# Optimization experiments

Measured on AMD Instinct MI355X. Metric: run time of the kernel, lower is better.

Reference implementation:

```python
import jax, jax.numpy as jnp
import numpy as np

B, N, E, DIN, DH = 32, 2000, 64000, 128, 128


def setup_inputs() -> dict:
    key = jax.random.key(0)
    ks = jax.random.split(key, 8)
    gene_emb = jax.random.normal(ks[0], (B, N, DIN), dtype=jnp.float32)
    edge_src = jax.random.randint(ks[1], (E,), 0, N, dtype=jnp.int32)
    edge_dst = jax.random.randint(ks[2], (E,), 0, N, dtype=jnp.int32)
    s1 = 1.0 / np.sqrt(DIN)
    s2 = 1.0 / np.sqrt(DH)
    W1 = jax.random.normal(ks[3], (DIN, DH), dtype=jnp.float32) * s1
    b1 = jnp.zeros((DH,), dtype=jnp.float32)
    W2 = jax.random.normal(ks[4], (DH, DH), dtype=jnp.float32) * s2
    b2 = jnp.zeros((DH,), dtype=jnp.float32)
    return {"gene_emb": gene_emb, "edge_src": edge_src, "edge_dst": edge_dst,
            "W1": W1, "b1": b1, "W2": W2, "b2": b2, "pathway_idx": 0}


def _gcn_conv(x, src, dst, norm_e, self_norm, W, b):
    # x: [B, N, Din] -> [B, N, Dout]; PyG GCNConv: linear first, then normalized aggregation
    h = jnp.einsum('bnd,de->bne', x, W)
    msgs = h[:, src, :] * norm_e[None, :, None]          # [B, E, Dout] gather
    agg = jax.vmap(lambda m: jax.ops.segment_sum(m, dst, num_segments=h.shape[1]))(msgs)
    # self-loop contribution (A+I): norm = dinv[i]^2
    return agg + h * self_norm[None, :, None] + b


def reference(gene_emb, edge_src, edge_dst, W1, b1, W2, b2, pathway_idx):
    n = gene_emb.shape[1]
    # symmetric GCN normalization with self loops: deg[i] = in_degree + 1
    deg = jnp.zeros((n,), dtype=gene_emb.dtype).at[edge_dst].add(1.0) + 1.0
    dinv = jax.lax.rsqrt(deg)
    norm_e = dinv[edge_src] * dinv[edge_dst]
    self_norm = dinv * dinv
    x = jax.nn.relu(_gcn_conv(gene_emb, edge_src, edge_dst, norm_e, self_norm, W1, b1))
    x = _gcn_conv(x, edge_src, edge_dst, norm_e, self_norm, W2, b2)
    # global_mean_pool over each graph copy (all graphs have n nodes)
    return jnp.mean(x, axis=1)  # [B, DH]
```

## Files before the change

### kernel.cpp

```cpp
#include <hip/hip_runtime.h>

namespace {
constexpr int NB = 32;
constexpr int NN = 2000;
constexpr int NE = 64000;
constexpr int ND = 128;
constexpr int TR = 16;
constexpr int NCHUNK = NN / TR;
constexpr int NXCD = 8;
constexpr int BPB = 2;
constexpr int PAIRS_PER_XCD = NB / (NXCD * BPB);
constexpr int NPAIR = NB / BPB;
constexpr int GRID_FUSED = NPAIR * NCHUNK;
constexpr int SL = 80;

constexpr int CVT_BLOCKS  = 1000;
constexpr int W_BLOCKS    = 8;
constexpr int EDGE_BLOCKS = 250;

constexpr size_t OFF_CNT    = 0;
constexpr size_t OFF_CNT2   = 8192;
constexpr size_t OFF_WSUM   = 16384;
constexpr size_t MEMSET_BYTES = 24576;
constexpr size_t OFF_SLOT2  = 24576;
constexpr size_t OFF_WF     = OFF_SLOT2 + (size_t)NN * SL * 8;
constexpr size_t OFF_YP     = OFF_WF + 32768;
constexpr size_t OFF_XBF    = OFF_YP + (size_t)NB * NCHUNK * ND * 4;

typedef __attribute__((ext_vector_type(8))) short bf16x8;
typedef __attribute__((ext_vector_type(4))) float f32x4;

__device__ __forceinline__ ushort f32_to_bf16(float f) {
    uint u = __float_as_uint(f);
    u += 0x7fffu + ((u >> 16) & 1u);
    return (ushort)(u >> 16);
}
__device__ __forceinline__ uint pack_bf16x2(float lo, float hi) {
    return (uint)f32_to_bf16(lo) | ((uint)f32_to_bf16(hi) << 16);
}
}

__global__ void k_prep1(const float* __restrict__ X, ushort* __restrict__ xbf,
                        const float* __restrict__ W1, uint* __restrict__ wf,
                        const int* __restrict__ dst, int* __restrict__ cnt) {
    const int blk = blockIdx.x;
    if (blk < CVT_BLOCKS) {
        const float4* __restrict__ X4 = (const float4*)X;
        ushort4* __restrict__ O4 = (ushort4*)xbf;
        const int base = blk * 2048 + (int)threadIdx.x;
        #pragma unroll
        for (int k = 0; k < 8; k++) {
            int i = base + k * 256;
            float4 v = X4[i];
            ushort4 o;
            o.x = f32_to_bf16(v.x);
            o.y = f32_to_bf16(v.y);
            o.z = f32_to_bf16(v.z);
            o.w = f32_to_bf16(v.w);
            O4[i] = o;
        }
    } else if (blk < CVT_BLOCKS + W_BLOCKS) {
        int g = (blk - CVT_BLOCKS) * 256 + threadIdx.x;
        int lane = g & 63, f = g >> 6;
        int nt = f >> 2, kc = f & 3;
        int col = nt * 16 + (lane & 15);
        int k0  = kc * 32 + (lane >> 4) * 8;
        uint4 o;
        o.x = pack_bf16x2(W1[(k0 + 0) * ND + col], W1[(k0 + 1) * ND + col]);
        o.y = pack_bf16x2(W1[(k0 + 2) * ND + col], W1[(k0 + 3) * ND + col]);
        o.z = pack_bf16x2(W1[(k0 + 4) * ND + col], W1[(k0 + 5) * ND + col]);
        o.w = pack_bf16x2(W1[(k0 + 6) * ND + col], W1[(k0 + 7) * ND + col]);
        ((uint4*)wf)[g] = o;
    } else {
        int e = (blk - CVT_BLOCKS - W_BLOCKS) * 256 + threadIdx.x;
        atomicAdd(&cnt[dst[e]], 1);
    }
}

__global__ void k_prep2(const int* __restrict__ src, const int* __restrict__ dst,
                        const int* __restrict__ cnt, int* __restrict__ cnt2,
                        float* __restrict__ wsum, int2* __restrict__ slot2) {
    int e = blockIdx.x * 256 + threadIdx.x;
    int s = src[e], d = dst[e];
    float w = rsqrtf((float)(cnt[s] + 1)) * rsqrtf((float)(cnt[d] + 1));
    int p = atomicAdd(&cnt2[d], 1);
    if (p < SL) slot2[(size_t)d * SL + p] = make_int2(s, __float_as_int(w));
    atomicAdd(&wsum[s], w);
}

__global__ __launch_bounds__(256, 4) void k_fused(const ushort* __restrict__ xbf,
                                                  const int* __restrict__ cnt,
                                                  const int2* __restrict__ slot2,
                                                  const float* __restrict__ wsum,
                                                  const uint* __restrict__ wfrag,
                                                  const float* __restrict__ b1,
                                                  float* __restrict__ ypart) {
    __shared__ __align__(16) uint AsU[2][TR * 68];
    __shared__ int2  sE[TR][SL];
    __shared__ float sDinv[TR];
    __shared__ float sWn[TR];
    __shared__ int   sCnt[TR];
    const int tid = threadIdx.x;

    const int L     = blockIdx.x;
    const int xcd   = L & (NXCD - 1);
    const int sl    = L >> 3;
    const int pair  = sl / NCHUNK;
    const int chunk = sl - pair * NCHUNK;
    const int b0    = xcd * (BPB * PAIRS_PER_XCD) + pair * BPB;
    const int n0    = chunk * TR;

    if (tid < TR) {
        int n = n0 + tid;
        int cr = cnt[n];
        float d = rsqrtf((float)(cr + 1));
        sCnt[tid]  = min(cr, SL);
        sDinv[tid] = d;
        sWn[tid]   = wsum[n] + d * d;
    }
    __syncthreads();

    const int wv = tid >> 6, ln = tid & 63;
    const int p = ln >> 5, col = ln & 31;
    const uint2* __restrict__ X0 = (const uint2*)(xbf + (size_t)b0 * NN * ND);
    const uint2* __restrict__ X1 = X0 + (size_t)NN * ND / 4;

    bf16x8 wfv[2][4];
    const bf16x8* Wf8 = (const bf16x8*)wfrag;
    #pragma unroll
    for (int nt2 = 0; nt2 < 2; nt2++)
        #pragma unroll
        for (int kc = 0; kc < 4; kc++)
            wfv[nt2][kc] = Wf8[(((2 * wv + nt2) * 4 + kc) * 64) + ln];

    #pragma unroll
    for (int ii = 0; ii < 4; ii++) {
        int j = wv * 4 + ii;
        int c = sCnt[j];
        const int2* sp = slot2 + (size_t)(n0 + j) * SL;
        for (int base = 0; base < c; base += 64)
            if (base + ln < c) sE[j][base + ln] = sp[base + ln];
    }

    #pragma unroll 1
    for (int ii = 0; ii < 4; ii++) {
        const int j = wv * 4 + ii;
        const int n = n0 + j;
        const int c = sCnt[j];
        float4 a  = {0.f, 0.f, 0.f, 0.f}, ab = a;
        float4 g  = a, gb = a;
        {
            uint2 q = X0[(size_t)p * (NN * ND / 4) + n * 32 + col];
            float sn = sDinv[j] * sDinv[j];
            float w0 = p ? 0.f : sn;
            float w1 = p ? sn : 0.f;
            float f0 = __uint_as_float(q.x << 16);
            float f1 = __uint_as_float(q.x & 0xffff0000u);
            float f2 = __uint_as_float(q.y << 16);
            float f3 = __uint_as_float(q.y & 0xffff0000u);
            a.x = w0 * f0; a.y = w0 * f1; a.z = w0 * f2; a.w = w0 * f3;
            g.x = w1 * f0; g.y = w1 * f1; g.z = w1 * f2; g.w = w1 * f3;
        }
        int e = 0;
        for (; e + 8 <= c; e += 8) {
            int sidx[4]; float w[4]; uint2 q0[4], q1[4];
            #pragma unroll
            for (int q = 0; q < 4; q++) {
                int2 ed = sE[j][e + 2 * q + p];
                sidx[q] = ed.x; w[q] = __int_as_float(ed.y);
            }
            #pragma unroll
            for (int q = 0; q < 4; q++) {
                int off = sidx[q] * 32 + col;
                q0[q] = X0[off];
                q1[q] = X1[off];
            }
            #pragma unroll
            for (int q = 0; q < 4; q++) {
                float f0 = __uint_as_float(q0[q].x << 16);
                float f1 = __uint_as_float(q0[q].x & 0xffff0000u);
                float f2 = __uint_as_float(q0[q].y << 16);
                float f3 = __uint_as_float(q0[q].y & 0xffff0000u);
                float h0 = __uint_as_float(q1[q].x << 16);
                float h1 = __uint_as_float(q1[q].x & 0xffff0000u);
                float h2 = __uint_as_float(q1[q].y << 16);
                float h3 = __uint_as_float(q1[q].y & 0xffff0000u);
                if (q & 1) {
                    ab.x = fmaf(w[q], f0, ab.x); ab.y = fmaf(w[q], f1, ab.y);
                    ab.z = fmaf(w[q], f2, ab.z); ab.w = fmaf(w[q], f3, ab.w);
                    gb.x = fmaf(w[q], h0, gb.x); gb.y = fmaf(w[q], h1, gb.y);
                    gb.z = fmaf(w[q], h2, gb.z); gb.w = fmaf(w[q], h3, gb.w);
                } else {
                    a.x = fmaf(w[q], f0, a.x); a.y = fmaf(w[q], f1, a.y);
                    a.z = fmaf(w[q], f2, a.z); a.w = fmaf(w[q], f3, a.w);
                    g.x = fmaf(w[q], h0, g.x); g.y = fmaf(w[q], h1, g.y);
                    g.z = fmaf(w[q], h2, g.z); g.w = fmaf(w[q], h3, g.w);
                }
            }
        }
        for (; e < c; e += 2) {
            int ee = e + p;
            int eidx = (ee < c) ? ee : e;
            int2 ed = sE[j][eidx];
            float w = (ee < c) ? __int_as_float(ed.y) : 0.f;
            int off = ed.x * 32 + col;
            uint2 u0 = X0[off], u1 = X1[off];
            a.x = fmaf(w, __uint_as_float(u0.x << 16), a.x);
            a.y = fmaf(w, __uint_as_float(u0.x & 0xffff0000u), a.y);
            a.z = fmaf(w, __uint_as_float(u0.y << 16), a.z);
            a.w = fmaf(w, __uint_as_float(u0.y & 0xffff0000u), a.w);
            g.x = fmaf(w, __uint_as_float(u1.x << 16), g.x);
            g.y = fmaf(w, __uint_as_float(u1.x & 0xffff0000u), g.y);
            g.z = fmaf(w, __uint_as_float(u1.y << 16), g.z);
            g.w = fmaf(w, __uint_as_float(u1.y & 0xffff0000u), g.w);
        }
        a.x += ab.x; a.y += ab.y; a.z += ab.z; a.w += ab.w;
        g.x += gb.x; g.y += gb.y; g.z += gb.z; g.w += gb.w;
        a.x += __shfl_xor(a.x, 32); a.y += __shfl_xor(a.y, 32);
        a.z += __shfl_xor(a.z, 32); a.w += __shfl_xor(a.w, 32);
        g.x += __shfl_xor(g.x, 32); g.y += __shfl_xor(g.y, 32);
        g.z += __shfl_xor(g.z, 32); g.w += __shfl_xor(g.w, 32);
        float4 av;
        av.x = p ? g.x : a.x; av.y = p ? g.y : a.y;
        av.z = p ? g.z : a.z; av.w = p ? g.w : a.w;
        AsU[p][j * 68 + 2 * col]     = pack_bf16x2(av.x, av.y);
        AsU[p][j * 68 + 2 * col + 1] = pack_bf16x2(av.z, av.w);
    }
    __syncthreads();

    const int lane15 = ln & 15, quad = ln >> 4;
    f32x4 zero4 = {0.f, 0.f, 0.f, 0.f};
    f32x4 acc[2][2];
    acc[0][0] = zero4; acc[0][1] = zero4; acc[1][0] = zero4; acc[1][1] = zero4;

    const bf16x8* A0 = (const bf16x8*)AsU[0];
    const bf16x8* A1 = (const bf16x8*)AsU[1];
    #pragma unroll
    for (int kc = 0; kc < 4; kc++) {
        bf16x8 af0 = A0[lane15 * 17 + kc * 4 + quad];
        bf16x8 af1 = A1[lane15 * 17 + kc * 4 + quad];
        #pragma unroll
        for (int nt2 = 0; nt2 < 2; nt2++) {
            acc[0][nt2] = __builtin_amdgcn_mfma_f32_16x16x32_bf16(
                af0, wfv[nt2][kc], acc[0][nt2], 0, 0, 0);
            acc[1][nt2] = __builtin_amdgcn_mfma_f32_16x16x32_bf16(
                af1, wfv[nt2][kc], acc[1][nt2], 0, 0, 0);
        }
    }

    #pragma unroll
    for (int nt2 = 0; nt2 < 2; nt2++) {
        int cg = (2 * wv + nt2) * 16 + lane15;
        float bias = b1[cg];
        #pragma unroll
        for (int b = 0; b < 2; b++) {
            float part = 0.f;
            #pragma unroll
            for (int r = 0; r < 4; r++)
                part = fmaf(sWn[quad * 4 + r], fmaxf(acc[b][nt2][r] + bias, 0.f), part);
            part += __shfl_xor(part, 16);
            part += __shfl_xor(part, 32);
            if (quad == 0)
                ypart[((size_t)(b0 + b) * NCHUNK + chunk) * ND + cg] = part;
        }
    }
}

__global__ __launch_bounds__(128) void k_out(const float* __restrict__ ypart,
                                             const float* __restrict__ W2,
                                             const float* __restrict__ b2,
                                             float* __restrict__ out) {
    __shared__ float ys[128];
    const int b = blockIdx.x;
    const int d = threadIdx.x;
    float s = 0.f;
    for (int c = 0; c < NCHUNK; c++)
        s += ypart[((size_t)b * NCHUNK + c) * ND + d];
    ys[d] = s * (1.f / (float)NN);
    __syncthreads();
    float acc = b2[d];
    #pragma unroll 8
    for (int k = 0; k < 128; k++)
        acc = fmaf(ys[k], W2[k * ND + d], acc);
    out[b * ND + d] = acc;
}

extern "C" void kernel_launch(void* const* d_in, const int* in_sizes, int n_in,
                              void* d_out, int out_size, void* d_ws, size_t ws_size,
                              hipStream_t stream) {
    (void)in_sizes; (void)n_in; (void)out_size; (void)ws_size;
    const float* X   = (const float*)d_in[0];
    const int*   src = (const int*)d_in[1];
    const int*   dst = (const int*)d_in[2];
    const float* W1  = (const float*)d_in[3];
    const float* b1  = (const float*)d_in[4];
    const float* W2  = (const float*)d_in[5];
    const float* b2  = (const float*)d_in[6];
    float* out = (float*)d_out;

    char* ws = (char*)d_ws;
    int*    cnt   = (int*)   (ws + OFF_CNT);
    int*    cnt2  = (int*)   (ws + OFF_CNT2);
    float*  wsum  = (float*) (ws + OFF_WSUM);
    int2*   slot2 = (int2*)  (ws + OFF_SLOT2);
    uint*   wfb   = (uint*)  (ws + OFF_WF);
    float*  ypart = (float*) (ws + OFF_YP);
    ushort* xbf   = (ushort*)(ws + OFF_XBF);

    (void)hipMemsetAsync(ws, 0, MEMSET_BYTES, stream);
    k_prep1<<<CVT_BLOCKS + W_BLOCKS + EDGE_BLOCKS, 256, 0, stream>>>(
        X, xbf, W1, wfb, dst, cnt);
    k_prep2<<<EDGE_BLOCKS, 256, 0, stream>>>(src, dst, cnt, cnt2, wsum, slot2);
    k_fused<<<GRID_FUSED, 256, 0, stream>>>(xbf, cnt, slot2, wsum, wfb, b1, ypart);
    k_out<<<NB, 128, 0, stream>>>(ypart, W2, b2, out);
}
```

Measured before the change: 169.0 us.

## Pack FMAs into float2 vectors, raise occupancy, remap conversion blocks per XCD

The gather-accumulate loop now uses two-wide float vector FMAs so the compiler can emit packed FMA instructions, which cuts VALU instruction count. The fused kernel's launch bounds go from 4 to 8 blocks per CU to allow more waves in flight for latency hiding, at the risk of register spills. The bf16 conversion blocks are remapped so each XCD handles a contiguous range of the input, and the input loads are made nontemporal.

```diff
diff --git a/kernel.cpp b/kernel.cpp
--- a/kernel.cpp
+++ b/kernel.cpp
@@ -29,6 +29,8 @@
 
 typedef __attribute__((ext_vector_type(8))) short bf16x8;
 typedef __attribute__((ext_vector_type(4))) float f32x4;
+typedef __attribute__((ext_vector_type(2))) float f32x2;
+typedef __attribute__((ext_vector_type(4))) ushort u16x4;
 
 __device__ __forceinline__ ushort f32_to_bf16(float f) {
     uint u = __float_as_uint(f);
@@ -37,6 +39,12 @@
 }
 __device__ __forceinline__ uint pack_bf16x2(float lo, float hi) {
     return (uint)f32_to_bf16(lo) | ((uint)f32_to_bf16(hi) << 16);
+}
+__device__ __forceinline__ f32x2 unpk2(uint u) {
+    f32x2 r;
+    r.x = __uint_as_float(u << 16);
+    r.y = __uint_as_float(u & 0xffff0000u);
+    return r;
 }
 }
 
@@ -45,14 +53,15 @@
                         const int* __restrict__ dst, int* __restrict__ cnt) {
     const int blk = blockIdx.x;
     if (blk < CVT_BLOCKS) {
-        const float4* __restrict__ X4 = (const float4*)X;
-        ushort4* __restrict__ O4 = (ushort4*)xbf;
-        const int base = blk * 2048 + (int)threadIdx.x;
+        const int xcd = blk & 7, m = blk >> 3;
+        const f32x4* __restrict__ X4 = (const f32x4*)X;
+        u16x4* __restrict__ O4 = (u16x4*)xbf;
+        const int base = (xcd * 125 + m) * 2048 + (int)threadIdx.x;
         #pragma unroll
         for (int k = 0; k < 8; k++) {
             int i = base + k * 256;
-            float4 v = X4[i];
-            ushort4 o;
+            f32x4 v = __builtin_nontemporal_load(&X4[i]);
+            u16x4 o;
             o.x = f32_to_bf16(v.x);
             o.y = f32_to_bf16(v.y);
             o.z = f32_to_bf16(v.z);
@@ -88,7 +97,7 @@
     atomicAdd(&wsum[s], w);
 }
 
-__global__ __launch_bounds__(256, 4) void k_fused(const ushort* __restrict__ xbf,
+__global__ __launch_bounds__(256, 8) void k_fused(const ushort* __restrict__ xbf,
                                                   const int* __restrict__ cnt,
                                                   const int2* __restrict__ slot2,
                                                   const float* __restrict__ wsum,
@@ -147,19 +156,17 @@
         const int j = wv * 4 + ii;
         const int n = n0 + j;
         const int c = sCnt[j];
-        float4 a  = {0.f, 0.f, 0.f, 0.f}, ab = a;
-        float4 g  = a, gb = a;
+        f32x2 z2 = {0.f, 0.f};
+        f32x2 aA01, aA23, gA01, gA23;
+        f32x2 aB01 = z2, aB23 = z2, gB01 = z2, gB23 = z2;
         {
             uint2 q = X0[(size_t)p * (NN * ND / 4) + n * 32 + col];
             float sn = sDinv[j] * sDinv[j];
             float w0 = p ? 0.f : sn;
             float w1 = p ? sn : 0.f;
-            float f0 = __uint_as_float(q.x << 16);
-            float f1 = __uint_as_float(q.x & 0xffff0000u);
-            float f2 = __uint_as_float(q.y << 16);
-            float f3 = __uint_as_float(q.y & 0xffff0000u);
-            a.x = w0 * f0; a.y = w0 * f1; a.z = w0 * f2; a.w = w0 * f3;
-            g.x = w1 * f0; g.y = w1 * f1; g.z = w1 * f2; g.w = w1 * f3;
+            f32x2 x01 = unpk2(q.x), x23 = unpk2(q.y);
+            aA01 = x01 * w0; aA23 = x23 * w0;
+            gA01 = x01 * w1; gA23 = x23 * w1;
         }
         int e = 0;
         for (; e + 8 <= c; e += 8) {
@@ -177,24 +184,19 @@
             }
             #pragma unroll
             for (int q = 0; q < 4; q++) {
-                float f0 = __uint_as_float(q0[q].x << 16);
-                float f1 = __uint_as_float(q0[q].x & 0xffff0000u);
-                float f2 = __uint_as_float(q0[q].y << 16);
-                float f3 = __uint_as_float(q0[q].y & 0xffff0000u);
-                float h0 = __uint_as_float(q1[q].x << 16);
-                float h1 = __uint_as_float(q1[q].x & 0xffff0000u);
-                float h2 = __uint_as_float(q1[q].y << 16);
-                float h3 = __uint_as_float(q1[q].y & 0xffff0000u);
+                f32x2 wq = {w[q], w[q]};
+                f32x2 x01 = unpk2(q0[q].x), x23 = unpk2(q0[q].y);
+                f32x2 y01 = unpk2(q1[q].x), y23 = unpk2(q1[q].y);
                 if (q & 1) {
-                    ab.x = fmaf(w[q], f0, ab.x); ab.y = fmaf(w[q], f1, ab.y);
-                    ab.z = fmaf(w[q], f2, ab.z); ab.w = fmaf(w[q], f3, ab.w);
-                    gb.x = fmaf(w[q], h0, gb.x); gb.y = fmaf(w[q], h1, gb.y);
-                    gb.z = fmaf(w[q], h2, gb.z); gb.w = fmaf(w[q], h3, gb.w);
+                    aB01 = __builtin_elementwise_fma(wq, x01, aB01);
+                    aB23 = __builtin_elementwise_fma(wq, x23, aB23);
+                    gB01 = __builtin_elementwise_fma(wq, y01, gB01);
+                    gB23 = __builtin_elementwise_fma(wq, y23, gB23);
                 } else {
-                    a.x = fmaf(w[q], f0, a.x); a.y = fmaf(w[q], f1, a.y);
-                    a.z = fmaf(w[q], f2, a.z); a.w = fmaf(w[q], f3, a.w);
-                    g.x = fmaf(w[q], h0, g.x); g.y = fmaf(w[q], h1, g.y);
-                    g.z = fmaf(w[q], h2, g.z); g.w = fmaf(w[q], h3, g.w);
+                    aA01 = __builtin_elementwise_fma(wq, x01, aA01);
+                    aA23 = __builtin_elementwise_fma(wq, x23, aA23);
+                    gA01 = __builtin_elementwise_fma(wq, y01, gA01);
+                    gA23 = __builtin_elementwise_fma(wq, y23, gA23);
                 }
             }
         }
@@ -202,29 +204,25 @@
             int ee = e + p;
             int eidx = (ee < c) ? ee : e;
             int2 ed = sE[j][eidx];
-            float w = (ee < c) ? __int_as_float(ed.y) : 0.f;
+            float ws = (ee < c) ? __int_as_float(ed.y) : 0.f;
+            f32x2 wq = {ws, ws};
             int off = ed.x * 32 + col;
             uint2 u0 = X0[off], u1 = X1[off];
-            a.x = fmaf(w, __uint_as_float(u0.x << 16), a.x);
-            a.y = fmaf(w, __uint_as_float(u0.x & 0xffff0000u), a.y);
-            a.z = fmaf(w, __uint_as_float(u0.y << 16), a.z);
-            a.w = fmaf(w, __uint_as_float(u0.y & 0xffff0000u), a.w);
-            g.x = fmaf(w, __uint_as_float(u1.x << 16), g.x);
-            g.y = fmaf(w, __uint_as_float(u1.x & 0xffff0000u), g.y);
-            g.z = fmaf(w, __uint_as_float(u1.y << 16), g.z);
-            g.w = fmaf(w, __uint_as_float(u1.y & 0xffff0000u), g.w);
-        }
-        a.x += ab.x; a.y += ab.y; a.z += ab.z; a.w += ab.w;
-        g.x += gb.x; g.y += gb.y; g.z += gb.z; g.w += gb.w;
-        a.x += __shfl_xor(a.x, 32); a.y += __shfl_xor(a.y, 32);
-        a.z += __shfl_xor(a.z, 32); a.w += __shfl_xor(a.w, 32);
-        g.x += __shfl_xor(g.x, 32); g.y += __shfl_xor(g.y, 32);
-        g.z += __shfl_xor(g.z, 32); g.w += __shfl_xor(g.w, 32);
-        float4 av;
-        av.x = p ? g.x : a.x; av.y = p ? g.y : a.y;
-        av.z = p ? g.z : a.z; av.w = p ? g.w : a.w;
-        AsU[p][j * 68 + 2 * col]     = pack_bf16x2(av.x, av.y);
-        AsU[p][j * 68 + 2 * col + 1] = pack_bf16x2(av.z, av.w);
+            aA01 = __builtin_elementwise_fma(wq, unpk2(u0.x), aA01);
+            aA23 = __builtin_elementwise_fma(wq, unpk2(u0.y), aA23);
+            gA01 = __builtin_elementwise_fma(wq, unpk2(u1.x), gA01);
+            gA23 = __builtin_elementwise_fma(wq, unpk2(u1.y), gA23);
+        }
+        aA01 += aB01; aA23 += aB23;
+        gA01 += gB01; gA23 += gB23;
+        aA01.x += __shfl_xor(aA01.x, 32); aA01.y += __shfl_xor(aA01.y, 32);
+        aA23.x += __shfl_xor(aA23.x, 32); aA23.y += __shfl_xor(aA23.y, 32);
+        gA01.x += __shfl_xor(gA01.x, 32); gA01.y += __shfl_xor(gA01.y, 32);
+        gA23.x += __shfl_xor(gA23.x, 32); gA23.y += __shfl_xor(gA23.y, 32);
+        f32x2 s01 = p ? gA01 : aA01;
+        f32x2 s23 = p ? gA23 : aA23;
+        AsU[p][j * 68 + 2 * col]     = pack_bf16x2(s01.x, s01.y);
+        AsU[p][j * 68 + 2 * col + 1] = pack_bf16x2(s23.x, s23.y);
     }
     __syncthreads();
 
```

Measured after the change: 187.8 us. +11.2%, slower.
